# Optimization experiments

Measured on AMD Instinct MI355X. Metric: run time of the kernel, lower is better.

Reference implementation:

```python
import jax, jax.numpy as jnp
import numpy as np

B, L, H, T_MAX, D_ID, D_SZ, D_POS = 64, 1024, 256, 128, 128, 64, 128
V_ID, V_SZ = 65536, 256


def setup_inputs() -> dict:
    key = jax.random.key(0)
    ks = jax.random.split(key, 16)
    s = 0.02
    inp = {
        'obj_id': jax.random.randint(ks[0], (B,), 0, V_ID, dtype=jnp.int32),
        'obj_size': jax.random.randint(ks[1], (B,), 0, V_SZ, dtype=jnp.int32),
        'cache_lines': jax.random.randint(ks[2], (B, L), 0, V_ID, dtype=jnp.int32),
        'lengths': jax.random.randint(ks[3], (B,), 0, L, dtype=jnp.int32),
        'c0': jax.random.normal(ks[4], (B, H), jnp.float32),
        'h0': jax.random.normal(ks[5], (B, H), jnp.float32),
        'history': jax.random.normal(ks[6], (B, T_MAX - 1, H), jnp.float32),
        # learned parameters
        'obj_id_table': jax.random.normal(ks[7], (V_ID, D_ID), jnp.float32) * s,
        'obj_size_table': jax.random.normal(ks[8], (V_SZ, D_SZ), jnp.float32) * s,
        'pos_table': jax.random.normal(ks[9], (T_MAX, D_POS), jnp.float32) * s,
        'W_ih': jax.random.normal(ks[10], (4 * H, D_ID + D_SZ), jnp.float32) * s,
        'W_hh': jax.random.normal(ks[11], (4 * H, H), jnp.float32) * s,
        'b_ih': jnp.zeros((4 * H,), jnp.float32),
        'b_hh': jnp.zeros((4 * H,), jnp.float32),
        'attn_W': jax.random.normal(ks[12], (D_ID, H), jnp.float32) * s,
        'scorer_W': jax.random.normal(ks[13], (1, H + D_POS), jnp.float32) * s,
        'scorer_b': jnp.zeros((1,), jnp.float32),
        'reuse_W': jax.random.normal(ks[14], (1, H + D_POS), jnp.float32) * s,
        'reuse_b': jnp.zeros((1,), jnp.float32),
    }
    return inp


def reference(obj_id, obj_size, cache_lines, lengths, c0, h0, history,
              obj_id_table, obj_size_table, pos_table,
              W_ih, W_hh, b_ih, b_hh, attn_W,
              scorer_W, scorer_b, reuse_W, reuse_b):
    # --- embed current access and run one LSTMCell step ---
    x = jnp.concatenate([obj_id_table[obj_id], obj_size_table[obj_size]], axis=-1)  # (B, D_ID+D_SZ)
    gates = x @ W_ih.T + b_ih + h0 @ W_hh.T + b_hh  # (B, 4H)
    i, f, g, o = jnp.split(gates, 4, axis=-1)
    c = jax.nn.sigmoid(f) * c0 + jax.nn.sigmoid(i) * jnp.tanh(g)
    h = jax.nn.sigmoid(o) * jnp.tanh(c)

    # --- growing hidden-state history (deque bounded at max_attention_history) ---
    hist = jnp.concatenate([history, h[:, None, :]], axis=1)  # (B, T, H)
    T = hist.shape[1]
    pos = jnp.broadcast_to(pos_table[:T][None], (hist.shape[0], T, pos_table.shape[1]))
    values = jnp.concatenate([hist, pos], axis=-1)  # (B, T, H+P)

    # --- cache line embeddings (cache_lines_embedder == obj_id_embedder) ---
    q = obj_id_table[cache_lines]  # (B, L, D_ID)

    # --- General (bilinear) multi-query attention over history ---
    scores = jnp.einsum('bld,dh,bth->blt', q, attn_W, hist)  # (B, L, T)
    weights = jax.nn.softmax(scores, axis=-1)
    contexts = jnp.einsum('blt,btv->blv', weights, values)  # (B, L, H+P)

    # --- heads ---
    line_scores = jax.nn.softmax((contexts @ scorer_W.T + scorer_b)[..., 0], axis=-1)  # (B, L)
    pred_reuse = (contexts @ reuse_W.T + reuse_b)[..., 0]  # (B, L)

    # --- mask_renormalize over valid (unpadded) cache lines ---
    valid = jnp.maximum(lengths, 1)[:, None]  # min_len=1 in pad()
    mask = (jnp.arange(line_scores.shape[1])[None, :] < valid).astype(line_scores.dtype)
    masked = line_scores * mask
    denom = masked.sum(axis=-1, keepdims=True)
    probs = masked / jnp.where(denom > 0, denom, 1.0)
    return probs, pred_reuse
```

## Files before the change

### kernel.cpp

```cpp
#include <hip/hip_runtime.h>
#include <math.h>

#define BB 64
#define LL 1024
#define HH 256
#define TT 128
#define D_ID 128
#define D_SZ 64
#define D_POS 128
#define DX 192

typedef short s16x8 __attribute__((ext_vector_type(8)));
typedef float f32x16 __attribute__((ext_vector_type(16)));
typedef unsigned short u16x8 __attribute__((ext_vector_type(8)));

__device__ __forceinline__ unsigned short f2bf(float f) {
    unsigned u = __float_as_uint(f);
    unsigned r = u + 0x7fffu + ((u >> 16) & 1u);
    return (unsigned short)(r >> 16);
}

__device__ __forceinline__ s16x8 pack8(float4 a, float4 b) {
    u16x8 p;
    p[0] = f2bf(a.x); p[1] = f2bf(a.y); p[2] = f2bf(a.z); p[3] = f2bf(a.w);
    p[4] = f2bf(b.x); p[5] = f2bf(b.y); p[6] = f2bf(b.z); p[7] = f2bf(b.w);
    return (s16x8)p;
}

__global__ void embed_kernel(const int* __restrict__ obj_id,
                             const int* __restrict__ obj_size,
                             const float* __restrict__ h0,
                             const float* __restrict__ obj_id_table,
                             const float* __restrict__ obj_size_table,
                             float* __restrict__ xh_t) {
    int tid = threadIdx.x;
    int b = tid & 63;
    int k = blockIdx.x * 4 + (tid >> 6);
    float v;
    if (k < D_ID)      v = obj_id_table[(size_t)obj_id[b] * D_ID + k];
    else if (k < DX)   v = obj_size_table[(size_t)obj_size[b] * D_SZ + (k - D_ID)];
    else               v = h0[b * HH + (k - DX)];
    xh_t[k * 64 + b] = v;
}

__global__ void gates_kernel(const float* __restrict__ xh_t,
                             const float* __restrict__ W_ih,
                             const float* __restrict__ W_hh,
                             const float* __restrict__ b_ih,
                             const float* __restrict__ b_hh,
                             const float* __restrict__ c0,
                             float* __restrict__ h_new) {
    int j = blockIdx.x;
    int tid = threadIdx.x;
    int b = tid & 63;
    int q = __builtin_amdgcn_readfirstlane(tid >> 6);
    int r = q * HH + j;
    __shared__ float gS[256];

    float acc = b_ih[r] + b_hh[r];
    const float* wi = W_ih + (size_t)r * DX;
    const float* wh = W_hh + (size_t)r * HH;
#pragma unroll 16
    for (int k = 0; k < DX; ++k)
        acc += wi[k] * xh_t[k * 64 + b];
#pragma unroll 16
    for (int k = 0; k < HH; ++k)
        acc += wh[k] * xh_t[(DX + k) * 64 + b];
    gS[q * 64 + b] = acc;
    __syncthreads();

    if (tid < 64) {
        float ig = 1.f / (1.f + expf(-gS[tid]));
        float fg = 1.f / (1.f + expf(-gS[64 + tid]));
        float gg = tanhf(gS[128 + tid]);
        float og = 1.f / (1.f + expf(-gS[192 + tid]));
        float c = fg * c0[tid * HH + j] + ig * gg;
        h_new[tid * HH + j] = og * tanhf(c);
    }
}

__global__ void proj_kernel(const float* __restrict__ history,
                            const float* __restrict__ h_new,
                            const float* __restrict__ attn_W,
                            unsigned short* __restrict__ hp) {
    int blk = blockIdx.x;
    int b  = blk >> 4;
    int t0 = ((blk >> 2) & 3) * 32;
    int d0 = (blk & 3) * 32;
    int lane = threadIdx.x;
    int ln = lane & 31, half = lane >> 5;

    int t = t0 + ln;
    const float* arow = (t < TT - 1)
        ? history + ((size_t)b * (TT - 1) + t) * HH
        : h_new + (size_t)b * HH;
    const float* brow = attn_W + (size_t)(d0 + ln) * HH;

    f32x16 acc;
#pragma unroll
    for (int r = 0; r < 16; ++r) acc[r] = 0.f;

#pragma unroll
    for (int ks = 0; ks < 16; ++ks) {
        int off = ks * 16 + half * 8;
        float4 a0 = *(const float4*)(arow + off);
        float4 a1 = *(const float4*)(arow + off + 4);
        float4 b0 = *(const float4*)(brow + off);
        float4 b1 = *(const float4*)(brow + off + 4);
        acc = __builtin_amdgcn_mfma_f32_32x32x16_bf16(
            pack8(a0, a1), pack8(b0, b1), acc, 0, 0, 0);
    }

#pragma unroll
    for (int r = 0; r < 16; ++r) {
        int tt = t0 + (r & 3) + 8 * (r >> 2) + 4 * half;
        hp[((size_t)b * TT + tt) * D_ID + d0 + ln] = f2bf(acc[r]);
    }
}

__global__ void svrv_kernel(const float* __restrict__ history,
                            const float* __restrict__ h_new,
                            const float* __restrict__ pos_table,
                            const float* __restrict__ scorer_W,
                            const float* __restrict__ reuse_W,
                            float* __restrict__ sv,
                            float* __restrict__ rv) {
    int b = blockIdx.x >> 1;
    int which = blockIdx.x & 1;
    int t = threadIdx.x;
    const float* w = which ? reuse_W : scorer_W;
    const float* hrow = (t < TT - 1)
        ? history + ((size_t)b * (TT - 1) + t) * HH
        : h_new + (size_t)b * HH;
    float acc = 0.f;
#pragma unroll 8
    for (int k = 0; k < HH / 4; ++k) {
        float4 hv = *(const float4*)(hrow + 4 * k);
        float4 wv = *(const float4*)(w + 4 * k);
        acc += hv.x * wv.x + hv.y * wv.y + hv.z * wv.z + hv.w * wv.w;
    }
    const float* prow = pos_table + (size_t)t * D_POS;
#pragma unroll 8
    for (int k = 0; k < D_POS / 4; ++k) {
        float4 pv = *(const float4*)(prow + 4 * k);
        float4 wv = *(const float4*)(w + HH + 4 * k);
        acc += pv.x * wv.x + pv.y * wv.y + pv.z * wv.z + pv.w * wv.w;
    }
    (which ? rv : sv)[b * TT + t] = acc;
}

__global__ void attn_kernel(const int* __restrict__ cache_lines,
                            const float* __restrict__ obj_id_table,
                            const unsigned short* __restrict__ hp,
                            const float* __restrict__ sv,
                            const float* __restrict__ rv,
                            const float* __restrict__ scorer_b,
                            const float* __restrict__ reuse_b,
                            float* __restrict__ logits,
                            float* __restrict__ out_reuse) {
    int b  = blockIdx.x >> 3;
    int l0 = (blockIdx.x & 7) * 128;
    int tid = threadIdx.x;
    __shared__ unsigned short qS[16384];
    __shared__ unsigned short hpS[16384];

    {
        int l = tid & 127;
        int cl = cache_lines[b * LL + l0 + l];
        const float* qrow = obj_id_table + (size_t)cl * D_ID;
        int lhi = (l >> 5) * 8, llo = l & 31;
#pragma unroll
        for (int i = 0; i < 8; ++i) {
            int u = 2 * i + (tid >> 7);
            float4 f0 = *(const float4*)(qrow + u * 8);
            float4 f1 = *(const float4*)(qrow + u * 8 + 4);
            *(s16x8*)(qS + (((lhi + (u >> 1)) * 64) + (u & 1) * 32 + llo) * 8) =
                pack8(f0, f1);
        }
    }
    {
        int t = tid & 127;
        const unsigned short* hrow = hp + ((size_t)b * TT + t) * D_ID;
        int thi = t >> 5, tlo = t & 31;
#pragma unroll
        for (int i = 0; i < 8; ++i) {
            int u = 2 * i + (tid >> 7);
            u16x8 p = *(const u16x8*)(hrow + u * 8);
            *(u16x8*)(hpS + ((((u >> 1) * 4 + thi) * 64) + (u & 1) * 32 + tlo) * 8) = p;
        }
    }
    __syncthreads();

    int w = tid >> 6;
    int lane = tid & 63;
    int ln = lane & 31, half = lane >> 5;

    f32x16 acc[4];
#pragma unroll
    for (int tt = 0; tt < 4; ++tt)
#pragma unroll
        for (int r = 0; r < 16; ++r) acc[tt][r] = 0.f;

    const unsigned short* qw = qS + w * 8 * 512;
#pragma unroll
    for (int k = 0; k < 8; ++k) {
        s16x8 a = *(const s16x8*)(qw + k * 512 + lane * 8);
#pragma unroll
        for (int tt = 0; tt < 4; ++tt) {
            s16x8 bf = *(const s16x8*)(hpS + (k * 4 + tt) * 512 + lane * 8);
            acc[tt] = __builtin_amdgcn_mfma_f32_32x32x16_bf16(a, bf, acc[tt], 0, 0, 0);
        }
    }

    float sv_r[4], rv_r[4];
#pragma unroll
    for (int tt = 0; tt < 4; ++tt) {
        sv_r[tt] = sv[b * TT + tt * 32 + ln];
        rv_r[tt] = rv[b * TT + tt * 32 + ln];
    }
    float sb = scorer_b[0], rb = reuse_b[0];

#pragma unroll
    for (int r = 0; r < 16; ++r) {
        float v0 = acc[0][r], v1 = acc[1][r], v2 = acc[2][r], v3 = acc[3][r];
        float m = fmaxf(fmaxf(v0, v1), fmaxf(v2, v3));
#pragma unroll
        for (int off = 1; off < 32; off <<= 1) m = fmaxf(m, __shfl_xor(m, off));
        float e0 = __expf(v0 - m), e1 = __expf(v1 - m),
              e2 = __expf(v2 - m), e3 = __expf(v3 - m);
        float s  = e0 + e1 + e2 + e3;
        float lg = e0 * sv_r[0] + e1 * sv_r[1] + e2 * sv_r[2] + e3 * sv_r[3];
        float rg = e0 * rv_r[0] + e1 * rv_r[1] + e2 * rv_r[2] + e3 * rv_r[3];
#pragma unroll
        for (int off = 1; off < 32; off <<= 1) {
            s  += __shfl_xor(s, off);
            lg += __shfl_xor(lg, off);
            rg += __shfl_xor(rg, off);
        }
        if (ln == 0) {
            int row = (r & 3) + 8 * (r >> 2) + 4 * half;
            int l = l0 + w * 32 + row;
            logits[b * LL + l] = lg / s + sb;
            out_reuse[b * LL + l] = rg / s + rb;
        }
    }
}

__global__ void finalsm_kernel(const float* __restrict__ logits,
                               const int* __restrict__ lengths,
                               float* __restrict__ out_probs) {
    int b = blockIdx.x;
    int tid = threadIdx.x;
    int valid = max(lengths[b], 1);
    float v[4];
    float m = -1e30f;
#pragma unroll
    for (int i = 0; i < 4; ++i) {
        int l = tid + 256 * i;
        v[i] = (l < valid) ? logits[b * LL + l] : -1e30f;
        m = fmaxf(m, v[i]);
    }
#pragma unroll
    for (int off = 1; off < 64; off <<= 1) m = fmaxf(m, __shfl_xor(m, off));
    __shared__ float redm[4];
    __shared__ float reds[4];
    int wave = tid >> 6;
    if ((tid & 63) == 0) redm[wave] = m;
    __syncthreads();
    m = fmaxf(fmaxf(redm[0], redm[1]), fmaxf(redm[2], redm[3]));
    float e[4];
    float s = 0.f;
#pragma unroll
    for (int i = 0; i < 4; ++i) {
        int l = tid + 256 * i;
        e[i] = (l < valid) ? expf(v[i] - m) : 0.f;
        s += e[i];
    }
#pragma unroll
    for (int off = 1; off < 64; off <<= 1) s += __shfl_xor(s, off);
    if ((tid & 63) == 0) reds[wave] = s;
    __syncthreads();
    s = reds[0] + reds[1] + reds[2] + reds[3];
    float inv = 1.f / s;
#pragma unroll
    for (int i = 0; i < 4; ++i)
        out_probs[b * LL + tid + 256 * i] = e[i] * inv;
}

extern "C" void kernel_launch(void* const* d_in, const int* in_sizes, int n_in,
                              void* d_out, int out_size, void* d_ws, size_t ws_size,
                              hipStream_t stream) {
    const int*   obj_id         = (const int*)d_in[0];
    const int*   obj_size       = (const int*)d_in[1];
    const int*   cache_lines    = (const int*)d_in[2];
    const int*   lengths        = (const int*)d_in[3];
    const float* c0             = (const float*)d_in[4];
    const float* h0             = (const float*)d_in[5];
    const float* history        = (const float*)d_in[6];
    const float* obj_id_table   = (const float*)d_in[7];
    const float* obj_size_table = (const float*)d_in[8];
    const float* pos_table      = (const float*)d_in[9];
    const float* W_ih           = (const float*)d_in[10];
    const float* W_hh           = (const float*)d_in[11];
    const float* b_ih           = (const float*)d_in[12];
    const float* b_hh           = (const float*)d_in[13];
    const float* attn_W         = (const float*)d_in[14];
    const float* scorer_W       = (const float*)d_in[15];
    const float* scorer_b       = (const float*)d_in[16];
    const float* reuse_W        = (const float*)d_in[17];
    const float* reuse_b        = (const float*)d_in[18];

    float* out = (float*)d_out;
    float* out_probs = out;
    float* out_reuse = out + BB * LL;

    char* ws = (char*)d_ws;
    float*          h_new  = (float*)(ws);
    unsigned short* hp     = (unsigned short*)(ws + 65536);
    float*          sv     = (float*)(ws + 65536 + 2097152);
    float*          rv     = (float*)(ws + 65536 + 2097152 + 32768);
    float*          xh_t   = (float*)(ws + 65536 + 2097152 + 65536);
    float*          logits = (float*)(ws + 65536 + 2097152 + 65536);

    hipLaunchKernelGGL(embed_kernel, dim3(112), dim3(256), 0, stream,
                       obj_id, obj_size, h0, obj_id_table, obj_size_table, xh_t);
    hipLaunchKernelGGL(gates_kernel, dim3(HH), dim3(256), 0, stream,
                       xh_t, W_ih, W_hh, b_ih, b_hh, c0, h_new);
    hipLaunchKernelGGL(proj_kernel, dim3(BB * 16), dim3(64), 0, stream,
                       history, h_new, attn_W, hp);
    hipLaunchKernelGGL(svrv_kernel, dim3(BB * 2), dim3(TT), 0, stream,
                       history, h_new, pos_table, scorer_W, reuse_W, sv, rv);
    hipLaunchKernelGGL(attn_kernel, dim3(BB * 8), dim3(256), 0, stream,
                       cache_lines, obj_id_table, hp, sv, rv,
                       scorer_b, reuse_b, logits, out_reuse);
    hipLaunchKernelGGL(finalsm_kernel, dim3(BB), dim3(256), 0, stream,
                       logits, lengths, out_probs);
}
```

Before: 165.8 us.

## Merge svrv into proj kernel and fuse final softmax via last-block counter

Folds the scorer/reuse value dot-products into extra blocks of the projection kernel, and folds the final masked softmax into the attention kernel: the last of the eight blocks per batch row, found with an atomic counter, does the row softmax. This drops two kernel launches and the gaps between them. In exchange it adds atomics, threadfences and a counter reset done inside the proj kernel. Overlap between the two slices is limited because the last block per row does the serial softmax work.

```diff
diff --git a/kernel.cpp b/kernel.cpp
--- a/kernel.cpp
+++ b/kernel.cpp
@@ -82,12 +82,48 @@
 __global__ void proj_kernel(const float* __restrict__ history,
                             const float* __restrict__ h_new,
                             const float* __restrict__ attn_W,
-                            unsigned short* __restrict__ hp) {
+                            const float* __restrict__ pos_table,
+                            const float* __restrict__ scorer_W,
+                            const float* __restrict__ reuse_W,
+                            unsigned short* __restrict__ hp,
+                            float* __restrict__ sv,
+                            float* __restrict__ rv,
+                            int* __restrict__ cnt) {
     int blk = blockIdx.x;
+    int tid = threadIdx.x;
+
+    if (blk >= BB * 16) {
+        int idx = blk - BB * 16;
+        if (idx == 0) cnt[tid] = 0;
+        int b = idx >> 2;
+        int which = (idx >> 1) & 1;
+        int t = (idx & 1) * 64 + tid;
+        const float* w = which ? reuse_W : scorer_W;
+        const float* hrow = (t < TT - 1)
+            ? history + ((size_t)b * (TT - 1) + t) * HH
+            : h_new + (size_t)b * HH;
+        float acc = 0.f;
+#pragma unroll 8
+        for (int k = 0; k < HH / 4; ++k) {
+            float4 hv = *(const float4*)(hrow + 4 * k);
+            float4 wv = *(const float4*)(w + 4 * k);
+            acc += hv.x * wv.x + hv.y * wv.y + hv.z * wv.z + hv.w * wv.w;
+        }
+        const float* prow = pos_table + (size_t)t * D_POS;
+#pragma unroll 8
+        for (int k = 0; k < D_POS / 4; ++k) {
+            float4 pv = *(const float4*)(prow + 4 * k);
+            float4 wv = *(const float4*)(w + HH + 4 * k);
+            acc += pv.x * wv.x + pv.y * wv.y + pv.z * wv.z + pv.w * wv.w;
+        }
+        (which ? rv : sv)[b * TT + t] = acc;
+        return;
+    }
+
     int b  = blk >> 4;
     int t0 = ((blk >> 2) & 3) * 32;
     int d0 = (blk & 3) * 32;
-    int lane = threadIdx.x;
+    int lane = tid;
     int ln = lane & 31, half = lane >> 5;
 
     int t = t0 + ln;
@@ -118,37 +154,6 @@
     }
 }
 
-__global__ void svrv_kernel(const float* __restrict__ history,
-                            const float* __restrict__ h_new,
-                            const float* __restrict__ pos_table,
-                            const float* __restrict__ scorer_W,
-                            const float* __restrict__ reuse_W,
-                            float* __restrict__ sv,
-                            float* __restrict__ rv) {
-    int b = blockIdx.x >> 1;
-    int which = blockIdx.x & 1;
-    int t = threadIdx.x;
-    const float* w = which ? reuse_W : scorer_W;
-    const float* hrow = (t < TT - 1)
-        ? history + ((size_t)b * (TT - 1) + t) * HH
-        : h_new + (size_t)b * HH;
-    float acc = 0.f;
-#pragma unroll 8
-    for (int k = 0; k < HH / 4; ++k) {
-        float4 hv = *(const float4*)(hrow + 4 * k);
-        float4 wv = *(const float4*)(w + 4 * k);
-        acc += hv.x * wv.x + hv.y * wv.y + hv.z * wv.z + hv.w * wv.w;
-    }
-    const float* prow = pos_table + (size_t)t * D_POS;
-#pragma unroll 8
-    for (int k = 0; k < D_POS / 4; ++k) {
-        float4 pv = *(const float4*)(prow + 4 * k);
-        float4 wv = *(const float4*)(w + HH + 4 * k);
-        acc += pv.x * wv.x + pv.y * wv.y + pv.z * wv.z + pv.w * wv.w;
-    }
-    (which ? rv : sv)[b * TT + t] = acc;
-}
-
 __global__ void attn_kernel(const int* __restrict__ cache_lines,
                             const float* __restrict__ obj_id_table,
                             const unsigned short* __restrict__ hp,
@@ -156,13 +161,19 @@
                             const float* __restrict__ rv,
                             const float* __restrict__ scorer_b,
                             const float* __restrict__ reuse_b,
+                            const int* __restrict__ lengths,
                             float* __restrict__ logits,
-                            float* __restrict__ out_reuse) {
+                            float* __restrict__ out_probs,
+                            float* __restrict__ out_reuse,
+                            int* __restrict__ cnt) {
     int b  = blockIdx.x >> 3;
     int l0 = (blockIdx.x & 7) * 128;
     int tid = threadIdx.x;
     __shared__ unsigned short qS[16384];
     __shared__ unsigned short hpS[16384];
+    __shared__ int lastFlag;
+    __shared__ float redm[4];
+    __shared__ float reds[4];
 
     {
         int l = tid & 127;
@@ -244,13 +255,14 @@
             out_reuse[b * LL + l] = rg / s + rb;
         }
     }
-}
-
-__global__ void finalsm_kernel(const float* __restrict__ logits,
-                               const int* __restrict__ lengths,
-                               float* __restrict__ out_probs) {
-    int b = blockIdx.x;
-    int tid = threadIdx.x;
+
+    __threadfence();
+    __syncthreads();
+    if (tid == 0) lastFlag = (atomicAdd(&cnt[b], 1) == 7);
+    __syncthreads();
+    if (!lastFlag) return;
+    __threadfence();
+
     int valid = max(lengths[b], 1);
     float v[4];
     float m = -1e30f;
@@ -262,8 +274,6 @@
     }
 #pragma unroll
     for (int off = 1; off < 64; off <<= 1) m = fmaxf(m, __shfl_xor(m, off));
-    __shared__ float redm[4];
-    __shared__ float reds[4];
     int wave = tid >> 6;
     if ((tid & 63) == 0) redm[wave] = m;
     __syncthreads();
@@ -321,18 +331,16 @@
     float*          rv     = (float*)(ws + 65536 + 2097152 + 32768);
     float*          xh_t   = (float*)(ws + 65536 + 2097152 + 65536);
     float*          logits = (float*)(ws + 65536 + 2097152 + 65536);
+    int*            cnt    = (int*)(ws + 65536 + 2097152 + 65536 + 262144);
 
     hipLaunchKernelGGL(embed_kernel, dim3(112), dim3(256), 0, stream,
                        obj_id, obj_size, h0, obj_id_table, obj_size_table, xh_t);
     hipLaunchKernelGGL(gates_kernel, dim3(HH), dim3(256), 0, stream,
                        xh_t, W_ih, W_hh, b_ih, b_hh, c0, h_new);
-    hipLaunchKernelGGL(proj_kernel, dim3(BB * 16), dim3(64), 0, stream,
-                       history, h_new, attn_W, hp);
-    hipLaunchKernelGGL(svrv_kernel, dim3(BB * 2), dim3(TT), 0, stream,
-                       history, h_new, pos_table, scorer_W, reuse_W, sv, rv);
+    hipLaunchKernelGGL(proj_kernel, dim3(BB * 16 + BB * 4), dim3(64), 0, stream,
+                       history, h_new, attn_W, pos_table, scorer_W, reuse_W,
+                       hp, sv, rv, cnt);
     hipLaunchKernelGGL(attn_kernel, dim3(BB * 8), dim3(256), 0, stream,
                        cache_lines, obj_id_table, hp, sv, rv,
-                       scorer_b, reuse_b, logits, out_reuse);
-    hipLaunchKernelGGL(finalsm_kernel, dim3(BB), dim3(256), 0, stream,
-                       logits, lengths, out_probs);
-}
+                       scorer_b, reuse_b, lengths, logits, out_probs, out_reuse, cnt);
+}
```

Result: slower. 215.2 us (+29.8%).
